# Kernel tuning notes

Measured on AMD Instinct MI355X. Metric: run time of the kernel, lower is better.

## Reference

```python
import jax, jax.numpy as jnp
import numpy as np

N, E, F_IN, H, G, K = 50000, 800000, 64, 200, 256, 3


def setup_inputs() -> dict:
    key = jax.random.key(0)
    ks = jax.random.split(key, 12)
    x = jax.random.normal(ks[0], (N, F_IN), jnp.float32)
    edge_index = jax.random.randint(ks[1], (2, E), 0, N, dtype=jnp.int64)
    batch = jnp.sort(jax.random.randint(ks[2], (N,), 0, G, dtype=jnp.int64))
    lmax = 1.5 + jax.random.uniform(ks[3], (G,), jnp.float32)  # per-graph lambda_max

    def lin(k, i, o):
        return (jax.random.normal(k, (K, i, o), jnp.float32) / np.sqrt(i)).astype(jnp.float32)

    return dict(
        x=x, edge_index=edge_index, batch=batch, lmax=lmax,
        W1=lin(ks[4], F_IN, H), b1=jnp.zeros((H,), jnp.float32),
        W2=lin(ks[5], H, H),    b2=jnp.zeros((H,), jnp.float32),
        W3=lin(ks[6], H, H),    b3=jnp.zeros((H,), jnp.float32),
        W4=lin(ks[7], H, H),    b4=jnp.zeros((H,), jnp.float32),
        fc_w=(jax.random.normal(ks[8], (2 * H, 2), jnp.float32) / np.sqrt(2 * H)).astype(jnp.float32),
        fc_b=jnp.zeros((2,), jnp.float32),
    )


def reference(x, edge_index, batch, lmax, W1, b1, W2, b2, W3, b3, W4, b4, fc_w, fc_b):
    n = x.shape[0]
    g = lmax.shape[0]
    src, dst = edge_index[0], edge_index[1]

    # PyG ChebConv sym normalization: L_hat = 2/lambda_max * (I - D^-1/2 A D^-1/2) - I
    deg = jax.ops.segment_sum(jnp.ones(src.shape[0], x.dtype), src, num_segments=n)
    dis = jnp.where(deg > 0, jnp.maximum(deg, 1.0) ** -0.5, 0.0)  # deg^{-1/2}, inf -> 0
    scale = 2.0 / lmax                                            # [G]
    w = -dis[src] * dis[dst] * scale[batch[src]]                  # off-diagonal edge weights [E]
    diag = scale[batch] - 1.0                                     # diagonal of L_hat, [N]

    def prop(h):  # L_hat @ h via sparse scatter
        return jax.ops.segment_sum(w[:, None] * h[src], dst, num_segments=n) + diag[:, None] * h

    def cheb(h, W, b):  # K=3 Chebyshev recurrence
        Tx0 = h
        Tx1 = prop(h)
        Tx2 = 2.0 * prop(Tx1) - Tx0
        return Tx0 @ W[0] + Tx1 @ W[1] + Tx2 @ W[2] + b

    h = jax.nn.relu(cheb(x, W1, b1))
    h = jax.nn.relu(cheb(h, W2, b2))
    h = jax.nn.relu(cheb(h, W3, b3))
    h = jax.nn.relu(cheb(h, W4, b4))

    cnt = jax.ops.segment_sum(jnp.ones(n, h.dtype), batch, num_segments=g)
    pooled_mean = jax.ops.segment_sum(h, batch, num_segments=g) / jnp.maximum(cnt, 1.0)[:, None]
    pooled_max = jax.ops.segment_max(h, batch, num_segments=g)
    z = jnp.concatenate([pooled_mean, pooled_max], axis=1) @ fc_w + fc_b
    return jax.nn.log_softmax(z, axis=1)
```

## Files before the change

kernel.cpp:

```cpp
#include <hip/hip_runtime.h>
#include <math.h>

#define NN 50000
#define MP 50048
#define NE 800000
#define FIN 64
#define HD 200
#define NG 256
#define SCAN_B 256
#define KPAD 224
#define NT 13
#define HB 12544
#define PER_B 3125

typedef _Float16 h16;
typedef __attribute__((ext_vector_type(8))) _Float16 half8;
typedef __attribute__((ext_vector_type(4))) float float4v;
typedef unsigned long long u64;

__global__ __launch_bounds__(256) void k_hist(const int* __restrict__ idx,
                                              unsigned* __restrict__ partial, int E) {
    __shared__ unsigned h[HB];
    int tid = threadIdx.x;
    int e0 = blockIdx.x * PER_B;
    int v[13];
#pragma unroll
    for (int j = 0; j < 13; ++j) {
        int o = j * 256 + tid;
        v[j] = (o < PER_B) ? idx[e0 + o] : -1;
    }
#pragma unroll
    for (int pass = 0; pass < 2; ++pass) {
        for (int t = tid; t < HB; t += 256) h[t] = 0;
        __syncthreads();
        int lo = pass * (2 * HB);
#pragma unroll
        for (int j = 0; j < 13; ++j) {
            int vv = v[j] - lo;
            if (vv >= 0 && vv < 2 * HB)
                atomicAdd(&h[vv >> 1], (vv & 1) ? 0x10000u : 1u);
        }
        __syncthreads();
        unsigned* pb = partial + ((size_t)pass * 256 + blockIdx.x) * HB;
        for (int t = tid; t < HB; t += 256) pb[t] = h[t];
        __syncthreads();
    }
}

__global__ void k_hreduce(const unsigned* __restrict__ partial, int* __restrict__ cnt, int n) {
    int i = blockIdx.x * blockDim.x + threadIdx.x;
    if (i >= 2 * HB) return;
    int pass = i / HB, p = i - pass * HB;
    const unsigned* pb = partial + (size_t)pass * 256 * HB + p;
    unsigned s = 0;
    for (int b = 0; b < 256; ++b) s += pb[(size_t)b * HB];
    int n0 = pass * 2 * HB + 2 * p;
    if (n0 < n)     cnt[n0]     = (int)(s & 0xffffu);
    if (n0 + 1 < n) cnt[n0 + 1] = (int)(s >> 16);
}

__global__ void k_node_prep(const int* __restrict__ degi, const int* __restrict__ batch,
                            const float* __restrict__ lmax, float* __restrict__ dis,
                            float* __restrict__ diag, int n) {
    int i = blockIdx.x * blockDim.x + threadIdx.x;
    if (i < n) {
        int d = degi[i];
        dis[i] = (d > 0) ? (1.0f / sqrtf((float)d)) : 0.0f;
        diag[i] = 2.0f / lmax[batch[i]] - 1.0f;
    }
}

__global__ void k_scan1(const int* __restrict__ cnt, int* __restrict__ excl,
                        int* __restrict__ bsum, int n) {
    __shared__ int sh[SCAN_B];
    int tid = threadIdx.x;
    int i = blockIdx.x * SCAN_B + tid;
    int v = (i < n) ? cnt[i] : 0;
    sh[tid] = v;
    __syncthreads();
    for (int off = 1; off < SCAN_B; off <<= 1) {
        int t = (tid >= off) ? sh[tid - off] : 0;
        __syncthreads();
        sh[tid] += t;
        __syncthreads();
    }
    if (i < n) excl[i] = sh[tid] - v;
    if (tid == SCAN_B - 1) bsum[blockIdx.x] = sh[tid];
}

__global__ void k_scan2(int* __restrict__ bsum, int nb) {
    __shared__ int sh[SCAN_B];
    int tid = threadIdx.x;
    int v = (tid < nb) ? bsum[tid] : 0;
    sh[tid] = v;
    __syncthreads();
    for (int off = 1; off < SCAN_B; off <<= 1) {
        int t = (tid >= off) ? sh[tid - off] : 0;
        __syncthreads();
        sh[tid] += t;
        __syncthreads();
    }
    if (tid < nb) bsum[tid] = sh[tid] - v;
}

__global__ void k_scan3(int* __restrict__ excl, const int* __restrict__ bsum, int n) {
    int i = blockIdx.x * SCAN_B + threadIdx.x;
    if (i < n) excl[i] += bsum[blockIdx.x];
}

__global__ void k_fillcsr(const int* __restrict__ src, const int* __restrict__ dst,
                          const int* __restrict__ batch, const float* __restrict__ lmax,
                          const float* __restrict__ dis, const int* __restrict__ rowstart,
                          int* __restrict__ fill, u64* __restrict__ csr, int E) {
    int e = blockIdx.x * blockDim.x + threadIdx.x;
    if (e < E) {
        int s = src[e], d = dst[e];
        int pos = rowstart[d] + atomicAdd(&fill[d], 1);
        float w = -dis[s] * dis[d] * (2.0f / lmax[batch[s]]);
        csr[pos] = (unsigned)s | ((u64)__float_as_uint(w) << 32);
    }
}

__global__ void k_split(const float* __restrict__ x, h16* __restrict__ x16, int total) {
    int i = blockIdx.x * blockDim.x + threadIdx.x;
    if (i < total) x16[i] = (h16)x[i];
}

__global__ void k_wprep(const float* __restrict__ W, h16* __restrict__ out,
                        int fin, int ksteps, int total) {
    int idx = blockIdx.x * blockDim.x + threadIdx.x;
    if (idx >= total) return;
    int kk = idx & 31;
    int r = idx >> 5;
    int nn = r % 208;
    int r2 = r / 208;
    int ks = r2 % ksteps;
    int seg = r2 / ksteps;
    int k = ks * 32 + kk;
    out[idx] = (nn < HD && k < fin) ? (h16)W[((size_t)seg * fin + k) * HD + nn] : (h16)0.f;
}

__global__ void k_bounds(const int* __restrict__ batch, int* __restrict__ gstart, int n) {
    int g = blockIdx.x * blockDim.x + threadIdx.x;
    if (g > NG) return;
    if (g == NG) { gstart[NG] = n; return; }
    int lo = 0, hi = n;
    while (lo < hi) {
        int mid = (lo + hi) >> 1;
        if (batch[mid] < g) lo = mid + 1; else hi = mid;
    }
    gstart[g] = lo;
}

__global__ __launch_bounds__(256) void k_gather(
    const int* __restrict__ rowstart, const int* __restrict__ rowcnt,
    const u64* __restrict__ csr, const float* __restrict__ diag,
    const h16* __restrict__ hin16, const h16* __restrict__ h016,
    h16* __restrict__ hout16, int s16, int lsh, int n, int mode) {
    int per = 256 >> lsh;
    int i = blockIdx.x * per + (threadIdx.x >> lsh);
    if (i >= n) return;
    int lane = threadIdx.x & ((1 << lsh) - 1);
    int c0 = lane * 4;
    if (c0 >= s16) return;
    int start = rowstart[i], cnt = rowcnt[i];
    float a0 = 0.f, a1 = 0.f, a2 = 0.f, a3 = 0.f;
    union U { uint2 u; h16 h[4]; };
    const u64* cp = csr + start;
    int k = 0;
    for (; k + 7 < cnt; k += 8) {
        u64 e[8];
#pragma unroll
        for (int j = 0; j < 8; ++j) e[j] = cp[k + j];
        U p[8];
#pragma unroll
        for (int j = 0; j < 8; ++j)
            p[j].u = *(const uint2*)(hin16 + (size_t)(unsigned)(e[j] & 0xffffffffu) * s16 + c0);
#pragma unroll
        for (int j = 0; j < 8; ++j) {
            float w = __uint_as_float((unsigned)(e[j] >> 32));
            a0 += w * (float)p[j].h[0];
            a1 += w * (float)p[j].h[1];
            a2 += w * (float)p[j].h[2];
            a3 += w * (float)p[j].h[3];
        }
    }
    for (; k + 1 < cnt; k += 2) {
        u64 e0 = cp[k], e1 = cp[k + 1];
        U p0, p1;
        p0.u = *(const uint2*)(hin16 + (size_t)(unsigned)(e0 & 0xffffffffu) * s16 + c0);
        p1.u = *(const uint2*)(hin16 + (size_t)(unsigned)(e1 & 0xffffffffu) * s16 + c0);
        float w0 = __uint_as_float((unsigned)(e0 >> 32));
        float w1 = __uint_as_float((unsigned)(e1 >> 32));
        a0 += w0 * (float)p0.h[0] + w1 * (float)p1.h[0];
        a1 += w0 * (float)p0.h[1] + w1 * (float)p1.h[1];
        a2 += w0 * (float)p0.h[2] + w1 * (float)p1.h[2];
        a3 += w0 * (float)p0.h[3] + w1 * (float)p1.h[3];
    }
    if (k < cnt) {
        u64 e0 = cp[k];
        U p0;
        p0.u = *(const uint2*)(hin16 + (size_t)(unsigned)(e0 & 0xffffffffu) * s16 + c0);
        float w0 = __uint_as_float((unsigned)(e0 >> 32));
        a0 += w0 * (float)p0.h[0];
        a1 += w0 * (float)p0.h[1];
        a2 += w0 * (float)p0.h[2];
        a3 += w0 * (float)p0.h[3];
    }
    float dg = diag[i];
    U hs; hs.u = *(const uint2*)(hin16 + (size_t)i * s16 + c0);
    float v0 = a0 + dg * (float)hs.h[0];
    float v1 = a1 + dg * (float)hs.h[1];
    float v2 = a2 + dg * (float)hs.h[2];
    float v3 = a3 + dg * (float)hs.h[3];
    if (mode == 1) {
        U h0; h0.u = *(const uint2*)(h016 + (size_t)i * s16 + c0);
        v0 = 2.f * v0 - (float)h0.h[0];
        v1 = 2.f * v1 - (float)h0.h[1];
        v2 = 2.f * v2 - (float)h0.h[2];
        v3 = 2.f * v3 - (float)h0.h[3];
    }
    U o;
    o.h[0] = (h16)v0; o.h[1] = (h16)v1; o.h[2] = (h16)v2; o.h[3] = (h16)v3;
    *(uint2*)(hout16 + (size_t)i * s16 + c0) = o.u;
}

__global__ __launch_bounds__(256) void k_gemm16(
    const h16* __restrict__ A0, const h16* __restrict__ A1, const h16* __restrict__ A2,
    int strideA, int ksteps,
    const h16* __restrict__ Wt, const float* __restrict__ bias,
    float* __restrict__ outF, h16* __restrict__ out16, int n) {
    int tid = threadIdx.x;
    int wave = tid >> 6, lane = tid & 63;
    int nq = lane & 15, quad = lane >> 4;
    int row0 = (blockIdx.x * 4 + wave) * 32;
    const h16* Aseg[3] = {A0, A1, A2};

    float4v acc[2][NT];
#pragma unroll
    for (int r = 0; r < 2; r++)
#pragma unroll
        for (int t = 0; t < NT; t++) acc[r][t] = (float4v)0.f;

    for (int seg = 0; seg < 3; ++seg) {
        const h16* Ab = Aseg[seg] + (size_t)(row0 + nq) * strideA + quad * 8;
        const h16* Bb = Wt + (size_t)seg * ksteps * 208 * 32 + (size_t)nq * 32 + quad * 8;
        for (int ks = 0; ks < ksteps; ++ks) {
            half8 af0 = *(const half8*)(Ab + ks * 32);
            half8 af1 = *(const half8*)(Ab + 16 * strideA + ks * 32);
            const h16* Bk = Bb + (size_t)ks * 208 * 32;
#pragma unroll
            for (int t = 0; t < NT; ++t) {
                half8 bf = *(const half8*)(Bk + t * 16 * 32);
                acc[0][t] = __builtin_amdgcn_mfma_f32_16x16x32_f16(af0, bf, acc[0][t], 0, 0, 0);
                acc[1][t] = __builtin_amdgcn_mfma_f32_16x16x32_f16(af1, bf, acc[1][t], 0, 0, 0);
            }
        }
    }
#pragma unroll
    for (int r = 0; r < 2; ++r) {
        int rowb = row0 + r * 16 + quad * 4;
#pragma unroll
        for (int t = 0; t < NT; ++t) {
            int col = t * 16 + nq;
            if (col >= HD) continue;
            float bj = bias[col];
#pragma unroll
            for (int g = 0; g < 4; ++g) {
                int row = rowb + g;
                if (row < n) {
                    float v = fmaxf(acc[r][t][g] + bj, 0.0f);
                    if (outF)  outF[(size_t)row * HD + col] = v;
                    if (out16) out16[(size_t)row * KPAD + col] = (h16)v;
                }
            }
        }
    }
}

__global__ __launch_bounds__(256) void k_pool_fc(
    const float* __restrict__ Hf, const int* __restrict__ gstart,
    const float* __restrict__ fcw, const float* __restrict__ fcb,
    float* __restrict__ out) {
    __shared__ float red[8];
    int g = blockIdx.x;
    int j = threadIdx.x;
    int i0 = gstart[g], i1 = gstart[g + 1];
    float s0 = 0.f, s1 = 0.f, s2 = 0.f, s3 = 0.f, mx = 0.f;
    if (j < HD) {
        int i = i0;
        for (; i + 3 < i1; i += 4) {
            float v0 = Hf[(size_t)i * HD + j];
            float v1 = Hf[(size_t)(i + 1) * HD + j];
            float v2 = Hf[(size_t)(i + 2) * HD + j];
            float v3 = Hf[(size_t)(i + 3) * HD + j];
            s0 += v0; s1 += v1; s2 += v2; s3 += v3;
            mx = fmaxf(mx, fmaxf(fmaxf(v0, v1), fmaxf(v2, v3)));
        }
        for (; i < i1; ++i) {
            float v = Hf[(size_t)i * HD + j];
            s0 += v; mx = fmaxf(mx, v);
        }
    }
    float cntf = (float)(i1 - i0);
    float mean = (s0 + s1 + s2 + s3) / fmaxf(cntf, 1.f);
    float p0 = 0.f, p1 = 0.f;
    if (j < HD) {
        p0 = mean * fcw[2 * j]     + mx * fcw[2 * (HD + j)];
        p1 = mean * fcw[2 * j + 1] + mx * fcw[2 * (HD + j) + 1];
    }
#pragma unroll
    for (int o = 32; o > 0; o >>= 1) {
        p0 += __shfl_down(p0, o);
        p1 += __shfl_down(p1, o);
    }
    int wave = j >> 6, lane = j & 63;
    if (lane == 0) { red[wave * 2] = p0; red[wave * 2 + 1] = p1; }
    __syncthreads();
    if (j == 0) {
        float z0 = red[0] + red[2] + red[4] + red[6] + fcb[0];
        float z1 = red[1] + red[3] + red[5] + red[7] + fcb[1];
        float m = fmaxf(z0, z1);
        float lse = m + logf(expf(z0 - m) + expf(z1 - m));
        out[g * 2 + 0] = z0 - lse;
        out[g * 2 + 1] = z1 - lse;
    }
}

extern "C" void kernel_launch(void* const* d_in, const int* in_sizes, int n_in,
                              void* d_out, int out_size, void* d_ws, size_t ws_size,
                              hipStream_t stream) {
    const float* x     = (const float*)d_in[0];
    const int*   edge  = (const int*)d_in[1];
    const int*   batch = (const int*)d_in[2];
    const float* lmax  = (const float*)d_in[3];
    const float* W1 = (const float*)d_in[4];  const float* b1 = (const float*)d_in[5];
    const float* W2 = (const float*)d_in[6];  const float* b2 = (const float*)d_in[7];
    const float* W3 = (const float*)d_in[8];  const float* b3 = (const float*)d_in[9];
    const float* W4 = (const float*)d_in[10]; const float* b4 = (const float*)d_in[11];
    const float* fcw = (const float*)d_in[12]; const float* fcb = (const float*)d_in[13];
    float* out = (float*)d_out;

    const int n = NN, E = NE;
    const int* src = edge;
    const int* dst = edge + E;

    float* ws = (float*)d_ws;
    size_t off = 0;
    auto alloc = [&](size_t nfloats) { float* p = ws + off; off += (nfloats + 3) & ~(size_t)3; return p; };
    int*   degi   = (int*)alloc(NN);
    float* dis    = alloc(NN);
    float* diag   = alloc(NN);
    int*   cntd   = (int*)alloc(NN);
    int*   rowst  = (int*)alloc(NN);
    int*   fill   = (int*)alloc(NN);
    int*   bsum   = (int*)alloc(SCAN_B);
    u64*   csr    = (u64*)alloc((size_t)NE * 2);
    int*   gstart = (int*)alloc(NG + 1);
    unsigned* hpart = (unsigned*)alloc((size_t)2 * 256 * HB);
    float* H      = alloc((size_t)MP * HD);
    h16*   x16    = (h16*)alloc((size_t)MP * FIN / 2);
    h16*   hi0    = (h16*)alloc((size_t)MP * KPAD / 2);
    h16*   hi1    = (h16*)alloc((size_t)MP * KPAD / 2);
    h16*   hi2    = (h16*)alloc((size_t)MP * KPAD / 2);
    const int WSZ0 = 3 * 2 * 208 * 32;
    const int WSZ  = 3 * 7 * 208 * 32;
    h16* wt0 = (h16*)alloc(WSZ0 / 2);
    h16* wt1 = (h16*)alloc(WSZ / 2);
    h16* wt2 = (h16*)alloc(WSZ / 2);
    h16* wt3 = (h16*)alloc(WSZ / 2);

    dim3 blk(256);
    int gE = (E + 255) / 256;
    int gN = (n + 255) / 256;
    int gScan = (n + SCAN_B - 1) / SCAN_B;
    int gGemm = MP / 128;
    int gHR = (2 * HB + 255) / 256;

    k_wprep<<<(WSZ0 + 255) / 256, blk, 0, stream>>>(W1, wt0, FIN, 2, WSZ0);
    k_wprep<<<(WSZ + 255) / 256, blk, 0, stream>>>(W2, wt1, HD, 7, WSZ);
    k_wprep<<<(WSZ + 255) / 256, blk, 0, stream>>>(W3, wt2, HD, 7, WSZ);
    k_wprep<<<(WSZ + 255) / 256, blk, 0, stream>>>(W4, wt3, HD, 7, WSZ);
    k_split<<<(NN * FIN + 255) / 256, blk, 0, stream>>>(x, x16, NN * FIN);
    k_bounds<<<2, blk, 0, stream>>>(batch, gstart, n);
    hipMemsetAsync(hi0, 0, (size_t)MP * KPAD * 2, stream);

    k_hist<<<256, blk, 0, stream>>>(src, hpart, E);
    k_hreduce<<<gHR, blk, 0, stream>>>(hpart, degi, n);
    k_hist<<<256, blk, 0, stream>>>(dst, hpart, E);
    k_hreduce<<<gHR, blk, 0, stream>>>(hpart, cntd, n);
    k_node_prep<<<gN, blk, 0, stream>>>(degi, batch, lmax, dis, diag, n);

    hipMemsetAsync(fill, 0, (size_t)NN * 4, stream);
    k_scan1<<<gScan, blk, 0, stream>>>(cntd, rowst, bsum, n);
    k_scan2<<<1, blk, 0, stream>>>(bsum, gScan);
    k_scan3<<<gScan, blk, 0, stream>>>(rowst, bsum, n);
    k_fillcsr<<<gE, blk, 0, stream>>>(src, dst, batch, lmax, dis, rowst, fill, csr, E);

    const h16* wt[4] = {wt0, wt1, wt2, wt3};
    const float* bl[4] = {b1, b2, b3, b4};
    for (int l = 0; l < 4; l++) {
        int s16 = (l == 0) ? FIN : KPAD;
        int lsh = (l == 0) ? 4 : 6;
        int per = 256 >> lsh;
        int gGat = (n + per - 1) / per;
        int ksteps = (l == 0) ? 2 : 7;
        const h16* a0 = (l == 0) ? x16 : hi0;
        k_gather<<<gGat, blk, 0, stream>>>(rowst, cntd, csr, diag, a0, a0, hi1, s16, lsh, n, 0);
        k_gather<<<gGat, blk, 0, stream>>>(rowst, cntd, csr, diag, hi1, a0, hi2, s16, lsh, n, 1);
        k_gemm16<<<gGemm, blk, 0, stream>>>(a0, hi1, hi2, s16, ksteps, wt[l], bl[l],
                                            (l == 3) ? H : nullptr,
                                            (l < 3) ? hi0 : nullptr, n);
    }

    k_pool_fc<<<NG, blk, 0, stream>>>(H, gstart, fcw, fcb, out);
}
```

Measured before the change: 851.5 us.

## Build CSR from per-block histogram scan and emit fp16 final layer output

Replaces the global-atomic CSR fill with a two-level counting sort: the per-block destination histograms are turned into exclusive per-block offsets, and each block ranks its edges with shared-memory atomics, which removes the fill memset and the contended global atomics. Per-node scale factors are precomputed so each edge weight needs two loads instead of four. The last GEMM now writes fp16 into an existing buffer and pooling reads fp16, which drops the fp32 H buffer and its writes. This adds some fp16 rounding in the pooled features and puts register pressure on the 13-element edge arrays.

After: 814.6 us. -4.3%, faster.

```diff
diff --git a/kernel.cpp b/kernel.cpp
--- a/kernel.cpp
+++ b/kernel.cpp
@@ -59,14 +59,33 @@
     if (n0 + 1 < n) cnt[n0 + 1] = (int)(s >> 16);
 }
 
+__global__ void k_hscan(unsigned* __restrict__ partial, int* __restrict__ cnt, int n) {
+    int i = blockIdx.x * blockDim.x + threadIdx.x;
+    if (i >= 2 * HB) return;
+    int pass = i / HB, p = i - pass * HB;
+    unsigned* pb = partial + (size_t)pass * 256 * HB + p;
+    unsigned run = 0;
+    for (int b = 0; b < 256; ++b) {
+        unsigned c = pb[(size_t)b * HB];
+        pb[(size_t)b * HB] = run;
+        run += c;
+    }
+    int n0 = pass * 2 * HB + 2 * p;
+    if (n0 < n)     cnt[n0]     = (int)(run & 0xffffu);
+    if (n0 + 1 < n) cnt[n0 + 1] = (int)(run >> 16);
+}
+
 __global__ void k_node_prep(const int* __restrict__ degi, const int* __restrict__ batch,
                             const float* __restrict__ lmax, float* __restrict__ dis,
-                            float* __restrict__ diag, int n) {
+                            float* __restrict__ qs, float* __restrict__ diag, int n) {
     int i = blockIdx.x * blockDim.x + threadIdx.x;
     if (i < n) {
         int d = degi[i];
-        dis[i] = (d > 0) ? (1.0f / sqrtf((float)d)) : 0.0f;
-        diag[i] = 2.0f / lmax[batch[i]] - 1.0f;
+        float di = (d > 0) ? (1.0f / sqrtf((float)d)) : 0.0f;
+        float sc = 2.0f / lmax[batch[i]];
+        dis[i] = di;
+        qs[i] = -di * sc;
+        diag[i] = sc - 1.0f;
     }
 }
 
@@ -108,16 +127,42 @@
     if (i < n) excl[i] += bsum[blockIdx.x];
 }
 
-__global__ void k_fillcsr(const int* __restrict__ src, const int* __restrict__ dst,
-                          const int* __restrict__ batch, const float* __restrict__ lmax,
-                          const float* __restrict__ dis, const int* __restrict__ rowstart,
-                          int* __restrict__ fill, u64* __restrict__ csr, int E) {
-    int e = blockIdx.x * blockDim.x + threadIdx.x;
-    if (e < E) {
-        int s = src[e], d = dst[e];
-        int pos = rowstart[d] + atomicAdd(&fill[d], 1);
-        float w = -dis[s] * dis[d] * (2.0f / lmax[batch[s]]);
-        csr[pos] = (unsigned)s | ((u64)__float_as_uint(w) << 32);
+__global__ __launch_bounds__(256) void k_fillcsr2(
+    const int* __restrict__ src, const int* __restrict__ dst,
+    const float* __restrict__ qs, const float* __restrict__ dis,
+    const int* __restrict__ rowst, const unsigned* __restrict__ hpart,
+    u64* __restrict__ csr, int E) {
+    __shared__ unsigned lrank[HB];
+    int tid = threadIdx.x;
+    int e0 = blockIdx.x * PER_B;
+    int vs[13], vd[13];
+#pragma unroll
+    for (int j = 0; j < 13; ++j) {
+        int o = j * 256 + tid;
+        vs[j] = (o < PER_B) ? src[e0 + o] : -1;
+        vd[j] = (o < PER_B) ? dst[e0 + o] : -1;
+    }
+#pragma unroll
+    for (int pass = 0; pass < 2; ++pass) {
+        for (int t = tid; t < HB; t += 256) lrank[t] = 0;
+        __syncthreads();
+        int lo = pass * (2 * HB);
+        const unsigned* base = hpart + ((size_t)pass * 256 + blockIdx.x) * HB;
+#pragma unroll
+        for (int j = 0; j < 13; ++j) {
+            int vv = vd[j] - lo;
+            if (vv >= 0 && vv < 2 * HB) {
+                unsigned old = atomicAdd(&lrank[vv >> 1], (vv & 1) ? 0x10000u : 1u);
+                unsigned rank = (vv & 1) ? (old >> 16) : (old & 0xffffu);
+                unsigned bs = base[vv >> 1];
+                unsigned b = (vv & 1) ? (bs >> 16) : (bs & 0xffffu);
+                int s = vs[j], d = vd[j];
+                int pos = rowst[d] + (int)b + (int)rank;
+                float w = qs[s] * dis[d];
+                csr[pos] = (unsigned)s | ((u64)__float_as_uint(w) << 32);
+            }
+        }
+        __syncthreads();
     }
 }
 
@@ -229,7 +274,7 @@
     const h16* __restrict__ A0, const h16* __restrict__ A1, const h16* __restrict__ A2,
     int strideA, int ksteps,
     const h16* __restrict__ Wt, const float* __restrict__ bias,
-    float* __restrict__ outF, h16* __restrict__ out16, int n) {
+    h16* __restrict__ out16, int n) {
     int tid = threadIdx.x;
     int wave = tid >> 6, lane = tid & 63;
     int nq = lane & 15, quad = lane >> 4;
@@ -268,18 +313,15 @@
 #pragma unroll
             for (int g = 0; g < 4; ++g) {
                 int row = rowb + g;
-                if (row < n) {
-                    float v = fmaxf(acc[r][t][g] + bj, 0.0f);
-                    if (outF)  outF[(size_t)row * HD + col] = v;
-                    if (out16) out16[(size_t)row * KPAD + col] = (h16)v;
-                }
+                if (row < n)
+                    out16[(size_t)row * KPAD + col] = (h16)fmaxf(acc[r][t][g] + bj, 0.0f);
             }
         }
     }
 }
 
 __global__ __launch_bounds__(256) void k_pool_fc(
-    const float* __restrict__ Hf, const int* __restrict__ gstart,
+    const h16* __restrict__ Hf, const int* __restrict__ gstart,
     const float* __restrict__ fcw, const float* __restrict__ fcb,
     float* __restrict__ out) {
     __shared__ float red[8];
@@ -290,15 +332,15 @@
     if (j < HD) {
         int i = i0;
         for (; i + 3 < i1; i += 4) {
-            float v0 = Hf[(size_t)i * HD + j];
-            float v1 = Hf[(size_t)(i + 1) * HD + j];
-            float v2 = Hf[(size_t)(i + 2) * HD + j];
-            float v3 = Hf[(size_t)(i + 3) * HD + j];
+            float v0 = (float)Hf[(size_t)i * KPAD + j];
+            float v1 = (float)Hf[(size_t)(i + 1) * KPAD + j];
+            float v2 = (float)Hf[(size_t)(i + 2) * KPAD + j];
+            float v3 = (float)Hf[(size_t)(i + 3) * KPAD + j];
             s0 += v0; s1 += v1; s2 += v2; s3 += v3;
             mx = fmaxf(mx, fmaxf(fmaxf(v0, v1), fmaxf(v2, v3)));
         }
         for (; i < i1; ++i) {
-            float v = Hf[(size_t)i * HD + j];
+            float v = (float)Hf[(size_t)i * KPAD + j];
             s0 += v; mx = fmaxf(mx, v);
         }
     }
@@ -350,15 +392,14 @@
     auto alloc = [&](size_t nfloats) { float* p = ws + off; off += (nfloats + 3) & ~(size_t)3; return p; };
     int*   degi   = (int*)alloc(NN);
     float* dis    = alloc(NN);
+    float* qs     = alloc(NN);
     float* diag   = alloc(NN);
     int*   cntd   = (int*)alloc(NN);
     int*   rowst  = (int*)alloc(NN);
-    int*   fill   = (int*)alloc(NN);
     int*   bsum   = (int*)alloc(SCAN_B);
     u64*   csr    = (u64*)alloc((size_t)NE * 2);
     int*   gstart = (int*)alloc(NG + 1);
     unsigned* hpart = (unsigned*)alloc((size_t)2 * 256 * HB);
-    float* H      = alloc((size_t)MP * HD);
     h16*   x16    = (h16*)alloc((size_t)MP * FIN / 2);
     h16*   hi0    = (h16*)alloc((size_t)MP * KPAD / 2);
     h16*   hi1    = (h16*)alloc((size_t)MP * KPAD / 2);
@@ -388,14 +429,13 @@
     k_hist<<<256, blk, 0, stream>>>(src, hpart, E);
     k_hreduce<<<gHR, blk, 0, stream>>>(hpart, degi, n);
     k_hist<<<256, blk, 0, stream>>>(dst, hpart, E);
-    k_hreduce<<<gHR, blk, 0, stream>>>(hpart, cntd, n);
-    k_node_prep<<<gN, blk, 0, stream>>>(degi, batch, lmax, dis, diag, n);
-
-    hipMemsetAsync(fill, 0, (size_t)NN * 4, stream);
+    k_hscan<<<gHR, blk, 0, stream>>>(hpart, cntd, n);
+    k_node_prep<<<gN, blk, 0, stream>>>(degi, batch, lmax, dis, qs, diag, n);
+
     k_scan1<<<gScan, blk, 0, stream>>>(cntd, rowst, bsum, n);
     k_scan2<<<1, blk, 0, stream>>>(bsum, gScan);
     k_scan3<<<gScan, blk, 0, stream>>>(rowst, bsum, n);
-    k_fillcsr<<<gE, blk, 0, stream>>>(src, dst, batch, lmax, dis, rowst, fill, csr, E);
+    k_fillcsr2<<<256, blk, 0, stream>>>(src, dst, qs, dis, rowst, hpart, csr, E);
 
     const h16* wt[4] = {wt0, wt1, wt2, wt3};
     const float* bl[4] = {b1, b2, b3, b4};
@@ -409,9 +449,8 @@
         k_gather<<<gGat, blk, 0, stream>>>(rowst, cntd, csr, diag, a0, a0, hi1, s16, lsh, n, 0);
         k_gather<<<gGat, blk, 0, stream>>>(rowst, cntd, csr, diag, hi1, a0, hi2, s16, lsh, n, 1);
         k_gemm16<<<gGemm, blk, 0, stream>>>(a0, hi1, hi2, s16, ksteps, wt[l], bl[l],
-                                            (l == 3) ? H : nullptr,
-                                            (l < 3) ? hi0 : nullptr, n);
-    }
-
-    k_pool_fc<<<NG, blk, 0, stream>>>(H, gstart, fcw, fcb, out);
-}
+                                            (l < 3) ? hi0 : hi1, n);
+    }
+
+    k_pool_fc<<<NG, blk, 0, stream>>>(hi1, gstart, fcw, fcb, out);
+}
```
